# Performance work log

Measured on AMD Instinct MI355X. Metric: run time of the kernel, lower is better.

The kernel has to match this reference:

```python
import jax, jax.numpy as jnp
import numpy as np

N_STEPS = 8  # fixed-step RK4 over t in [0, 1]


def setup_inputs() -> dict:
    key = jax.random.key(0)
    ks = jax.random.split(key, 5)
    B, T, F, C = 64, 4096, 76, 15
    x = jax.random.normal(ks[0], (B, T, F), dtype=jnp.float32)
    # Conv1d(76->76, k=3) weights, PyTorch OIH layout, fan-in scaled
    conv_w = jax.random.normal(ks[1], (F, F, 3), dtype=jnp.float32) * (1.0 / np.sqrt(F * 3))
    conv_b = jax.random.normal(ks[2], (F,), dtype=jnp.float32) * 0.01
    final_w = jax.random.normal(ks[3], (C, F), dtype=jnp.float32) * (1.0 / np.sqrt(F))
    final_b = jax.random.normal(ks[4], (C,), dtype=jnp.float32) * 0.01
    return {"x": x, "conv_w": conv_w, "conv_b": conv_b,
            "final_w": final_w, "final_b": final_b}


def _func(h, conv_w, conv_b):
    # h: [B, F, T]; Conv1d k=3 pad=1 -> Tanh (the ODE vector field)
    y = jax.lax.conv_general_dilated(
        h, conv_w, window_strides=(1,), padding=[(1, 1)],
        dimension_numbers=("NCH", "OIH", "NCH"))
    return jnp.tanh(y + conv_b[None, :, None])


def reference(x, conv_w, conv_b, final_w, final_b):
    # x: [B, T, F] -> permute to channels-first for Conv1d
    h0 = jnp.transpose(x, (0, 2, 1))  # [B, F, T]
    dt = jnp.float32(1.0 / N_STEPS)

    def rk4_step(h, _):
        k1 = _func(h, conv_w, conv_b)
        k2 = _func(h + 0.5 * dt * k1, conv_w, conv_b)
        k3 = _func(h + 0.5 * dt * k2, conv_w, conv_b)
        k4 = _func(h + dt * k3, conv_w, conv_b)
        return h + (dt / 6.0) * (k1 + 2.0 * k2 + 2.0 * k3 + k4), None

    hT, _ = jax.lax.scan(rk4_step, h0, None, length=N_STEPS)
    # back to [B, T, F], then final Linear(F -> num_classes)
    out = jnp.einsum("bft,cf->btc", hT, final_w) + final_b
    return out
```

## Files before the change

kernel.cpp:

```cpp
#include <hip/hip_runtime.h>
#include <cstdint>
#include <cstddef>

#define F_CH 76
#define T_LEN 4096
#define B_TOT 64
#define C_CLS 15
#define NSTEP 8

#define W_OUT  48
#define HALO2  8
#define NBT    86
#define NKB    5
#define SSTR   88
#define SROWS  66
#define TPB    384
#define HP     80

#define C2LOG2E 2.8853900817779268f

typedef __attribute__((ext_vector_type(8)))  __bf16 bf16x8;
typedef __attribute__((ext_vector_type(4)))  __bf16 bf16x4;
typedef __attribute__((ext_vector_type(16))) float  f32x16;

__global__ __launch_bounds__(256) void pad_copy_kernel(
    const float* __restrict__ x, float* __restrict__ h, int b0)
{
    int bl = blockIdx.y;
    int q  = blockIdx.x * 256 + threadIdx.x;
    int t  = q / 20, c4 = (q - t * 20) * 4;
    float4 v = {0.f, 0.f, 0.f, 0.f};
    if (c4 < F_CH)
        v = *(const float4*)(x + ((size_t)(b0 + bl) * T_LEN + t) * F_CH + c4);
    *(float4*)(h + ((size_t)bl * T_LEN + t) * HP + c4) = v;
}

__global__ __launch_bounds__(256) void wprep_kernel(
    const float* __restrict__ cw, __bf16* __restrict__ wpb)
{
    int idx = blockIdx.x * 256 + threadIdx.x;
    if (idx >= 3 * 96 * SSTR) return;
    int tap = idx / (96 * SSTR);
    int rem = idx - tap * 96 * SSTR;
    int c = rem / SSTR, ci = rem - c * SSTR;
    float v = 0.0f;
    if (c < F_CH && ci < F_CH) v = cw[((size_t)c * F_CH + ci) * 3 + tap];
    wpb[idx] = (__bf16)v;
}

__global__ __launch_bounds__(TPB, 4) void rk4_step2_kernel(
    const float* __restrict__ hin, float* __restrict__ hout,
    const __bf16* __restrict__ wpb, const float* __restrict__ cb)
{
    __shared__ __bf16 s_lds[2][SROWS][SSTR];
    __shared__ float  cb_lds[96];

    const int b    = blockIdx.y;
    const int T0   = blockIdx.x * W_OUT;
    const int tid  = threadIdx.x;
    const int lane = tid & 63;
    const int l31  = lane & 31;
    const int l5   = lane >> 5;
    const int wv   = tid >> 6;
    const int ct   = wv >> 1;
    const int tq   = wv & 1;

    const int  rb  = tq * 32 + l31;
    const int  tg  = T0 - HALO2 + rb;
    const bool tok = (tg >= 0 && tg < T_LEN);

    if (tid < 176) {
        int bi = tid / 88, rr = (tid % 88) / 44, c = tid % 44;
        ((uint32_t*)&s_lds[bi][rr ? (SROWS - 1) : 0][0])[c] = 0u;
    }
    if (tid < 96) cb_lds[tid] = (tid < F_CH) ? cb[tid] * C2LOG2E : 0.0f;

    float  hn[16];
    bf16x4 hpk[4];
    const float* hb = hin + (size_t)b * T_LEN * HP;
    #pragma unroll
    for (int q = 0; q < 4; ++q) {
        int c0 = ct * 32 + l5 * 4 + q * 8;
        float4 v = {0.f, 0.f, 0.f, 0.f};
        if (tok && c0 < HP) v = *(const float4*)(hb + (size_t)tg * HP + c0);
        hn[q*4+0]=v.x; hn[q*4+1]=v.y; hn[q*4+2]=v.z; hn[q*4+3]=v.w;
        hpk[q][0]=(__bf16)v.x; hpk[q][1]=(__bf16)v.y;
        hpk[q][2]=(__bf16)v.z; hpk[q][3]=(__bf16)v.w;
    }

    bf16x8 afr[3][NKB];
    #pragma unroll
    for (int tap = 0; tap < 3; ++tap)
        #pragma unroll
        for (int kb = 0; kb < NKB; ++kb)
            afr[tap][kb] = *(const bf16x8*)&wpb[((size_t)tap * 96 + ct * 32 + l31) * SSTR
                                                + kb * 16 + l5 * 8];

    const float dt = 0.125f;

    #pragma unroll 1
    for (int st = 0; st < 2; ++st) {
        #pragma unroll
        for (int q = 0; q < 4; ++q) {
            int c0 = ct * 32 + l5 * 4 + q * 8;
            if (c0 < HP) *(bf16x4*)&s_lds[0][rb + 1][c0] = hpk[q];
        }
        __syncthreads();

        #pragma unroll 1
        for (int e = 0; e < 4; ++e) {
            const float we   = (e == 0 || e == 3) ? dt / 6.0f : dt / 3.0f;
            const float al   = (e == 2) ? dt : 0.5f * dt;
            const float al_t = tok ? al : 0.0f;

            const __bf16 (*sb)[SSTR] = s_lds[e & 1];
            f32x16 a0 = {};
            #pragma unroll
            for (int tap = 0; tap < 3; ++tap) {
                #pragma unroll
                for (int kb = 0; kb < NKB; ++kb) {
                    bf16x8 bf = *(const bf16x8*)&sb[rb + tap][kb * 16 + l5 * 8];
                    a0 = __builtin_amdgcn_mfma_f32_32x32x16_bf16(afr[tap][kb], bf, a0, 0, 0, 0);
                }
            }

            __bf16 (*sw)[SSTR] = s_lds[(e + 1) & 1];
            #pragma unroll
            for (int q = 0; q < 4; ++q) {
                int c0 = ct * 32 + l5 * 4 + q * 8;
                if (c0 >= HP) continue;
                bf16x4 p;
                #pragma unroll
                for (int j = 0; j < 4; ++j) {
                    float y  = fmaf(a0[q*4+j], C2LOG2E, cb_lds[c0 + j]);
                    float ex = __builtin_amdgcn_exp2f(y);
                    float kv = fmaf(-2.0f, __builtin_amdgcn_rcpf(ex + 1.0f), 1.0f);
                    hn[q*4+j] = fmaf(we, kv, hn[q*4+j]);
                    if (e < 3) p[j] = (__bf16)fmaf(al_t, kv, (float)hpk[q][j]);
                }
                if (e < 3) *(bf16x4*)&sw[rb + 1][c0] = p;
            }
            if (e < 3) __syncthreads();
        }

        if (st == 0) {
            #pragma unroll
            for (int i = 0; i < 16; ++i) hn[i] = tok ? hn[i] : 0.0f;
            #pragma unroll
            for (int q = 0; q < 4; ++q)
                #pragma unroll
                for (int j = 0; j < 4; ++j) hpk[q][j] = (__bf16)hn[q*4+j];
            __syncthreads();
        }
    }

    if (rb >= HALO2 && rb < HALO2 + W_OUT && tg < T_LEN) {
        float* ho = hout + ((size_t)b * T_LEN + tg) * HP;
        #pragma unroll
        for (int q = 0; q < 4; ++q) {
            int c0 = ct * 32 + l5 * 4 + q * 8;
            if (c0 < HP) {
                float4 v;
                v.x = hn[q*4+0]; v.y = hn[q*4+1];
                v.z = hn[q*4+2]; v.w = hn[q*4+3];
                *(float4*)(ho + c0) = v;
            }
        }
    }
}

__global__ __launch_bounds__(256) void final_kernel(
    const float* __restrict__ h, const float* __restrict__ fw,
    const float* __restrict__ fb, float* __restrict__ out, int b0)
{
    int bl = blockIdx.y;
    int t  = blockIdx.x * 256 + threadIdx.x;
    const float* hr = h + ((size_t)bl * T_LEN + t) * HP;
    float acc[C_CLS];
#pragma unroll
    for (int c = 0; c < C_CLS; ++c) acc[c] = fb[c];
#pragma unroll
    for (int qf = 0; qf < 19; ++qf) {
        float4 v = *(const float4*)(hr + qf * 4);
#pragma unroll
        for (int c = 0; c < C_CLS; ++c) {
            const float* w = fw + c * F_CH + qf * 4;
            acc[c] = fmaf(w[0], v.x, acc[c]);
            acc[c] = fmaf(w[1], v.y, acc[c]);
            acc[c] = fmaf(w[2], v.z, acc[c]);
            acc[c] = fmaf(w[3], v.w, acc[c]);
        }
    }
    float* ob = out + ((size_t)(b0 + bl) * T_LEN + t) * C_CLS;
#pragma unroll
    for (int c = 0; c < C_CLS; ++c) ob[c] = acc[c];
}

extern "C" void kernel_launch(void* const* d_in, const int* in_sizes, int n_in,
                              void* d_out, int out_size, void* d_ws, size_t ws_size,
                              hipStream_t stream)
{
    const float* x  = (const float*)d_in[0];
    const float* cw = (const float*)d_in[1];
    const float* cb = (const float*)d_in[2];
    const float* fw = (const float*)d_in[3];
    const float* fb = (const float*)d_in[4];
    float* out = (float*)d_out;

    const size_t FT = (size_t)T_LEN * HP;

    __bf16* WPB = (__bf16*)d_ws;
    const size_t wpbFloats = 12800;
    float* planes = (float*)d_ws + wpbFloats;

    size_t planeBytes = 2 * FT * sizeof(float);
    size_t avail = ws_size - wpbFloats * sizeof(float);
    int Bc = (int)(avail / planeBytes);
    if (Bc > B_TOT) Bc = B_TOT;
    if (Bc < 1) Bc = 1;

    float* H0 = planes;
    float* H1 = H0 + (size_t)Bc * FT;

    wprep_kernel<<<(3 * 96 * SSTR + 255) / 256, 256, 0, stream>>>(cw, WPB);

    for (int b0 = 0; b0 < B_TOT; b0 += Bc) {
        int bc = (B_TOT - b0 < Bc) ? (B_TOT - b0) : Bc;

        dim3 gP(T_LEN * 20 / 256, bc);
        pad_copy_kernel<<<gP, 256, 0, stream>>>(x, H0, b0);

        float* hcur = H0;
        float* hnxt = H1;
        dim3 gR(NBT, bc);
        for (int st2 = 0; st2 < NSTEP / 2; ++st2) {
            rk4_step2_kernel<<<gR, TPB, 0, stream>>>(hcur, hnxt, WPB, cb);
            float* tmp = hcur; hcur = hnxt; hnxt = tmp;
        }

        dim3 gF(T_LEN / 256, bc);
        final_kernel<<<gF, 256, 0, stream>>>(hcur, fw, fb, out, b0);
    }
}
```

Measured before the change: 885.3 us.

## Widen time tile to 112 with 768-thread blocks and XOR-swizzled LDS layout

Each block now covers 128 time rows (112 outputs plus halo) using 12 waves instead of 64 rows with 6 waves. This cuts the fraction of redundant halo recompute and reduces the block count. The LDS activation buffer is also reorganised into 128-element rows with an XOR swizzle on 16-byte chunks, meant to avoid bank conflicts on the MFMA B-operand reads and the bf16x4 writes. The cost is larger blocks with more LDS each, which lowers occupancy and coarsens the tail across 37x64 blocks.

Result: faster. 818.0 us (-7.6%).

```diff
diff --git a/kernel.cpp b/kernel.cpp
--- a/kernel.cpp
+++ b/kernel.cpp
@@ -8,13 +8,14 @@
 #define C_CLS 15
 #define NSTEP 8
 
-#define W_OUT  48
+#define W_OUT  112
 #define HALO2  8
-#define NBT    86
+#define NBT    37
 #define NKB    5
-#define SSTR   88
-#define SROWS  66
-#define TPB    384
+#define WSTR   88
+#define SST    128
+#define SROWS  130
+#define TPB    768
 #define HP     80
 
 #define C2LOG2E 2.8853900817779268f
@@ -22,6 +23,10 @@
 typedef __attribute__((ext_vector_type(8)))  __bf16 bf16x8;
 typedef __attribute__((ext_vector_type(4)))  __bf16 bf16x4;
 typedef __attribute__((ext_vector_type(16))) float  f32x16;
+
+__device__ __forceinline__ int sw_off(int r, int v) {
+    return r * SST + (((v) ^ (r & 7)) << 3);
+}
 
 __global__ __launch_bounds__(256) void pad_copy_kernel(
     const float* __restrict__ x, float* __restrict__ h, int b0)
@@ -39,20 +44,20 @@
     const float* __restrict__ cw, __bf16* __restrict__ wpb)
 {
     int idx = blockIdx.x * 256 + threadIdx.x;
-    if (idx >= 3 * 96 * SSTR) return;
-    int tap = idx / (96 * SSTR);
-    int rem = idx - tap * 96 * SSTR;
-    int c = rem / SSTR, ci = rem - c * SSTR;
+    if (idx >= 3 * 96 * WSTR) return;
+    int tap = idx / (96 * WSTR);
+    int rem = idx - tap * 96 * WSTR;
+    int c = rem / WSTR, ci = rem - c * WSTR;
     float v = 0.0f;
     if (c < F_CH && ci < F_CH) v = cw[((size_t)c * F_CH + ci) * 3 + tap];
     wpb[idx] = (__bf16)v;
 }
 
-__global__ __launch_bounds__(TPB, 4) void rk4_step2_kernel(
+__global__ __launch_bounds__(TPB, 3) void rk4_step2_kernel(
     const float* __restrict__ hin, float* __restrict__ hout,
     const __bf16* __restrict__ wpb, const float* __restrict__ cb)
 {
-    __shared__ __bf16 s_lds[2][SROWS][SSTR];
+    __shared__ __bf16 s_lds[2][SROWS * SST];
     __shared__ float  cb_lds[96];
 
     const int b    = blockIdx.y;
@@ -62,16 +67,16 @@
     const int l31  = lane & 31;
     const int l5   = lane >> 5;
     const int wv   = tid >> 6;
-    const int ct   = wv >> 1;
-    const int tq   = wv & 1;
+    const int ct   = wv >> 2;
+    const int tq   = wv & 3;
 
     const int  rb  = tq * 32 + l31;
     const int  tg  = T0 - HALO2 + rb;
     const bool tok = (tg >= 0 && tg < T_LEN);
 
-    if (tid < 176) {
-        int bi = tid / 88, rr = (tid % 88) / 44, c = tid % 44;
-        ((uint32_t*)&s_lds[bi][rr ? (SROWS - 1) : 0][0])[c] = 0u;
+    if (tid < 256) {
+        int bi = tid / 128, rr = (tid % 128) / 64, c = tid % 64;
+        ((uint32_t*)&s_lds[bi][(rr ? (SROWS - 1) : 0) * SST])[c] = 0u;
     }
     if (tid < 96) cb_lds[tid] = (tid < F_CH) ? cb[tid] * C2LOG2E : 0.0f;
 
@@ -93,7 +98,7 @@
     for (int tap = 0; tap < 3; ++tap)
         #pragma unroll
         for (int kb = 0; kb < NKB; ++kb)
-            afr[tap][kb] = *(const bf16x8*)&wpb[((size_t)tap * 96 + ct * 32 + l31) * SSTR
+            afr[tap][kb] = *(const bf16x8*)&wpb[((size_t)tap * 96 + ct * 32 + l31) * WSTR
                                                 + kb * 16 + l5 * 8];
 
     const float dt = 0.125f;
@@ -103,7 +108,8 @@
         #pragma unroll
         for (int q = 0; q < 4; ++q) {
             int c0 = ct * 32 + l5 * 4 + q * 8;
-            if (c0 < HP) *(bf16x4*)&s_lds[0][rb + 1][c0] = hpk[q];
+            if (c0 < HP)
+                *(bf16x4*)&s_lds[0][sw_off(rb + 1, ct * 4 + q) + l5 * 4] = hpk[q];
         }
         __syncthreads();
 
@@ -113,18 +119,18 @@
             const float al   = (e == 2) ? dt : 0.5f * dt;
             const float al_t = tok ? al : 0.0f;
 
-            const __bf16 (*sb)[SSTR] = s_lds[e & 1];
+            const __bf16* sb = s_lds[e & 1];
             f32x16 a0 = {};
             #pragma unroll
             for (int tap = 0; tap < 3; ++tap) {
                 #pragma unroll
                 for (int kb = 0; kb < NKB; ++kb) {
-                    bf16x8 bf = *(const bf16x8*)&sb[rb + tap][kb * 16 + l5 * 8];
+                    bf16x8 bf = *(const bf16x8*)&sb[sw_off(rb + tap, kb * 2 + l5)];
                     a0 = __builtin_amdgcn_mfma_f32_32x32x16_bf16(afr[tap][kb], bf, a0, 0, 0, 0);
                 }
             }
 
-            __bf16 (*sw)[SSTR] = s_lds[(e + 1) & 1];
+            __bf16* sw = s_lds[(e + 1) & 1];
             #pragma unroll
             for (int q = 0; q < 4; ++q) {
                 int c0 = ct * 32 + l5 * 4 + q * 8;
@@ -138,7 +144,8 @@
                     hn[q*4+j] = fmaf(we, kv, hn[q*4+j]);
                     if (e < 3) p[j] = (__bf16)fmaf(al_t, kv, (float)hpk[q][j]);
                 }
-                if (e < 3) *(bf16x4*)&sw[rb + 1][c0] = p;
+                if (e < 3)
+                    *(bf16x4*)&sw[sw_off(rb + 1, ct * 4 + q) + l5 * 4] = p;
             }
             if (e < 3) __syncthreads();
         }
@@ -222,7 +229,7 @@
     float* H0 = planes;
     float* H1 = H0 + (size_t)Bc * FT;
 
-    wprep_kernel<<<(3 * 96 * SSTR + 255) / 256, 256, 0, stream>>>(cw, WPB);
+    wprep_kernel<<<(3 * 96 * WSTR + 255) / 256, 256, 0, stream>>>(cw, WPB);
 
     for (int b0 = 0; b0 < B_TOT; b0 += Bc) {
         int bc = (B_TOT - b0 < Bc) ? (B_TOT - b0) : Bc;
```
